# Performance work log

Measured on AMD Instinct MI355X. Metric: run time of the kernel, lower is better.

The kernel has to match this reference:

```python
import jax, jax.numpy as jnp
import numpy as np

DIM = 128

def setup_inputs() -> dict:
    key = jax.random.key(0)
    ks = jax.random.split(key, 4)
    N, C, L = 64, DIM, 4096
    scale = 1.0 / np.sqrt(DIM)
    return {
        "x": jax.random.normal(ks[0], (N, C, L), dtype=jnp.float32),
        "Wq": jax.random.normal(ks[1], (DIM, DIM), dtype=jnp.float32) * scale,
        "bq": jnp.zeros((DIM,), dtype=jnp.float32),
        "Wk": jax.random.normal(ks[2], (DIM, DIM), dtype=jnp.float32) * scale,
        "bk": jnp.zeros((DIM,), dtype=jnp.float32),
        "Wv": jax.random.normal(ks[3], (DIM, DIM), dtype=jnp.float32) * scale,
        "bv": jnp.zeros((DIM,), dtype=jnp.float32),
    }

def reference(x, Wq, bq, Wk, bk, Wv, bv):
    # x: [N, C, L] -> rearrange to [N, L, C]
    h = jnp.transpose(x, (0, 2, 1))                       # [N, L, C]
    q = jnp.einsum('nlc,cd->nld', h, Wq) + bq             # [N, L, D]
    k = jnp.einsum('nlc,cd->nld', h, Wk) + bk             # [N, L, D]
    v = jnp.einsum('nlc,cd->nld', h, Wv) + bv             # [N, L, D]
    # AFT-Simple: softmax over sequence axis of K, global weighted pool of V
    w = jax.nn.softmax(k, axis=1)                         # [N, L, D]
    pooled = jnp.sum(w * v, axis=1, keepdims=True)        # [N, 1, D]
    out = jax.nn.sigmoid(q) * pooled                      # [N, L, D]
    return jnp.transpose(out, (0, 2, 1))                  # [N, C, L]
```

## Files before the change

kernel.cpp:

```cpp
#include <hip/hip_runtime.h>
#include <hip/hip_bf16.h>

#define NB 64
#define CD 128
#define LL 4096
#define LCHUNK 64
#define NSUB 4
#define P1_NBLK 16
#define P3_NCHUNK 64

typedef __attribute__((ext_vector_type(8))) short short8;
typedef __attribute__((ext_vector_type(4))) float f32x4;

#define WT_OFF   0
#define WSM_OFF  131072
#define WSS_OFF  (WSM_OFF + NB*P1_NBLK*CD*4)
#define WSP_OFF  (WSS_OFF + NB*P1_NBLK*CD*4)
#define POOL_OFF (WSP_OFF + NB*P1_NBLK*CD*4)

__device__ __forceinline__ unsigned short f2bf(float f) {
    union { float f; unsigned u; } v; v.f = f;
    unsigned r = v.u + 0x7FFFu + ((v.u >> 16) & 1u);
    return (unsigned short)(r >> 16);
}

__global__ void prep_wt(const float* __restrict__ Wq, const float* __restrict__ Wk,
                        const float* __restrict__ Wv, unsigned short* __restrict__ wt) {
    int t = blockIdx.x >> 7;
    int d = blockIdx.x & 127;
    const float* W = (t == 0) ? Wq : (t == 1) ? Wk : Wv;
    int c = threadIdx.x;
    wt[((size_t)t*CD + d)*CD + c] = f2bf(W[c*CD + d]);
}

__global__ __launch_bounds__(256, 2)
void aft_pass1(const float* __restrict__ x, const unsigned short* __restrict__ wt,
               const float* __restrict__ bk, const float* __restrict__ bv,
               float* __restrict__ wsM, float* __restrict__ wsS, float* __restrict__ wsP) {
    __shared__ unsigned short lds_x[LCHUNK * 136];
    const int tid = threadIdx.x;
    const int n = blockIdx.x >> 4;
    const int blk = blockIdx.x & 15;
    const int w = tid >> 6, lane = tid & 63, r = lane & 15, g = lane >> 4;

    short8 a_k[2][4], a_v[2][4];
#pragma unroll
    for (int rt = 0; rt < 2; ++rt)
#pragma unroll
        for (int s = 0; s < 4; ++s) {
            int d = 32*w + 16*rt + r;
            a_k[rt][s] = *(const short8*)(wt + ((size_t)(1*CD + d))*CD + 32*s + 8*g);
            a_v[rt][s] = *(const short8*)(wt + ((size_t)(2*CD + d))*CD + 32*s + 8*g);
        }

    f32x4 bkv[2], bvv[2];
#pragma unroll
    for (int rt = 0; rt < 2; ++rt) {
        bkv[rt] = *(const f32x4*)(bk + 32*w + 16*rt + 4*g);
        bvv[rt] = *(const f32x4*)(bv + 32*w + 16*rt + 4*g);
    }

    float m_run[2][4], s_run[2][4], p_run[2][4];
#pragma unroll
    for (int rt = 0; rt < 2; ++rt)
#pragma unroll
        for (int v = 0; v < 4; ++v) { m_run[rt][v] = -1e30f; s_run[rt][v] = 0.f; p_run[rt][v] = 0.f; }

    for (int sub = 0; sub < NSUB; ++sub) {
        const int l0 = (blk*NSUB + sub) * LCHUNK;
        __syncthreads();
        {
            const int cc = tid >> 4, f = tid & 15;
#pragma unroll
            for (int it = 0; it < 8; ++it) {
                int c = cc + 16*it;
                f32x4 xv = *(const f32x4*)(x + ((size_t)n*CD + c)*LL + l0 + 4*f);
                int l = 4*f;
                lds_x[(l+0)*136 + c] = f2bf(xv[0]);
                lds_x[(l+1)*136 + c] = f2bf(xv[1]);
                lds_x[(l+2)*136 + c] = f2bf(xv[2]);
                lds_x[(l+3)*136 + c] = f2bf(xv[3]);
            }
        }
        __syncthreads();

        f32x4 acc_k[2][4], acc_v[2][4];
#pragma unroll
        for (int rt = 0; rt < 2; ++rt)
#pragma unroll
            for (int ct = 0; ct < 4; ++ct) {
                acc_k[rt][ct] = (f32x4){0.f,0.f,0.f,0.f};
                acc_v[rt][ct] = (f32x4){0.f,0.f,0.f,0.f};
            }

#pragma unroll
        for (int s = 0; s < 4; ++s) {
#pragma unroll
            for (int ct = 0; ct < 4; ++ct) {
                short8 b = *(const short8*)(lds_x + (ct*16 + r)*136 + 32*s + 8*g);
                acc_k[0][ct] = __builtin_amdgcn_mfma_f32_16x16x32_bf16(a_k[0][s], b, acc_k[0][ct], 0,0,0);
                acc_k[1][ct] = __builtin_amdgcn_mfma_f32_16x16x32_bf16(a_k[1][s], b, acc_k[1][ct], 0,0,0);
                acc_v[0][ct] = __builtin_amdgcn_mfma_f32_16x16x32_bf16(a_v[0][s], b, acc_v[0][ct], 0,0,0);
                acc_v[1][ct] = __builtin_amdgcn_mfma_f32_16x16x32_bf16(a_v[1][s], b, acc_v[1][ct], 0,0,0);
            }
        }

#pragma unroll
        for (int rt = 0; rt < 2; ++rt) {
#pragma unroll
            for (int v = 0; v < 4; ++v) {
                float k0 = acc_k[rt][0][v] + bkv[rt][v];
                float k1 = acc_k[rt][1][v] + bkv[rt][v];
                float k2 = acc_k[rt][2][v] + bkv[rt][v];
                float k3 = acc_k[rt][3][v] + bkv[rt][v];
                float v0 = acc_v[rt][0][v] + bvv[rt][v];
                float v1 = acc_v[rt][1][v] + bvv[rt][v];
                float v2 = acc_v[rt][2][v] + bvv[rt][v];
                float v3 = acc_v[rt][3][v] + bvv[rt][v];
                float m = fmaxf(fmaxf(k0,k1), fmaxf(k2,k3));
                m = fmaxf(m, __shfl_xor(m, 1, 64));
                m = fmaxf(m, __shfl_xor(m, 2, 64));
                m = fmaxf(m, __shfl_xor(m, 4, 64));
                m = fmaxf(m, __shfl_xor(m, 8, 64));
                float e0 = __expf(k0 - m), e1 = __expf(k1 - m);
                float e2 = __expf(k2 - m), e3 = __expf(k3 - m);
                float sl = (e0 + e1) + (e2 + e3);
                float pl = e0*v0 + e1*v1 + e2*v2 + e3*v3;
                sl += __shfl_xor(sl, 1, 64); pl += __shfl_xor(pl, 1, 64);
                sl += __shfl_xor(sl, 2, 64); pl += __shfl_xor(pl, 2, 64);
                sl += __shfl_xor(sl, 4, 64); pl += __shfl_xor(pl, 4, 64);
                sl += __shfl_xor(sl, 8, 64); pl += __shfl_xor(pl, 8, 64);
                float mo = m_run[rt][v];
                float mn = fmaxf(mo, m);
                float au = __expf(mo - mn);
                float bu = __expf(m - mn);
                s_run[rt][v] = s_run[rt][v]*au + sl*bu;
                p_run[rt][v] = p_run[rt][v]*au + pl*bu;
                m_run[rt][v] = mn;
            }
        }
    }

    if (r == 0) {
#pragma unroll
        for (int rt = 0; rt < 2; ++rt)
#pragma unroll
            for (int v = 0; v < 4; ++v) {
                int d = 32*w + 16*rt + 4*g + v;
                size_t idx = ((size_t)n*P1_NBLK + blk)*CD + d;
                wsM[idx] = m_run[rt][v];
                wsS[idx] = s_run[rt][v];
                wsP[idx] = p_run[rt][v];
            }
    }
}

__global__ void aft_pass2(const float* __restrict__ wsM, const float* __restrict__ wsS,
                          const float* __restrict__ wsP, float* __restrict__ pooled) {
    int n = blockIdx.x, d = threadIdx.x;
    float m = -1e30f, s = 0.f, p = 0.f;
    for (int b = 0; b < P1_NBLK; ++b) {
        size_t idx = ((size_t)n*P1_NBLK + b)*CD + d;
        float mb = wsM[idx], sb = wsS[idx], pb = wsP[idx];
        float mn = fmaxf(m, mb);
        float au = __expf(m - mn), bu = __expf(mb - mn);
        s = s*au + sb*bu;
        p = p*au + pb*bu;
        m = mn;
    }
    pooled[(size_t)n*CD + d] = p / s;
}

__global__ __launch_bounds__(256, 2)
void aft_pass3(const float* __restrict__ x, const unsigned short* __restrict__ wt,
               const float* __restrict__ bq, const float* __restrict__ pooled,
               float* __restrict__ out) {
    __shared__ unsigned short lds_x[LCHUNK * 136];
    __shared__ float lds_o[CD * 68];
    const int tid = threadIdx.x;
    const int n = blockIdx.x >> 6;
    const int ch = blockIdx.x & 63;
    const int l0 = ch * LCHUNK;
    const int w = tid >> 6, lane = tid & 63, r = lane & 15, g = lane >> 4;

    short8 a_q[2][4];
#pragma unroll
    for (int rt = 0; rt < 2; ++rt)
#pragma unroll
        for (int s = 0; s < 4; ++s) {
            int d = 32*w + 16*rt + r;
            a_q[rt][s] = *(const short8*)(wt + ((size_t)(0*CD + d))*CD + 32*s + 8*g);
        }

    {
        const int cc = tid >> 4, f = tid & 15;
#pragma unroll
        for (int it = 0; it < 8; ++it) {
            int c = cc + 16*it;
            f32x4 xv = *(const f32x4*)(x + ((size_t)n*CD + c)*LL + l0 + 4*f);
            int l = 4*f;
            lds_x[(l+0)*136 + c] = f2bf(xv[0]);
            lds_x[(l+1)*136 + c] = f2bf(xv[1]);
            lds_x[(l+2)*136 + c] = f2bf(xv[2]);
            lds_x[(l+3)*136 + c] = f2bf(xv[3]);
        }
    }
    __syncthreads();

    f32x4 acc[2][4];
#pragma unroll
    for (int rt = 0; rt < 2; ++rt)
#pragma unroll
        for (int ct = 0; ct < 4; ++ct) acc[rt][ct] = (f32x4){0.f,0.f,0.f,0.f};

#pragma unroll
    for (int s = 0; s < 4; ++s) {
#pragma unroll
        for (int ct = 0; ct < 4; ++ct) {
            short8 b = *(const short8*)(lds_x + (ct*16 + r)*136 + 32*s + 8*g);
            acc[0][ct] = __builtin_amdgcn_mfma_f32_16x16x32_bf16(a_q[0][s], b, acc[0][ct], 0,0,0);
            acc[1][ct] = __builtin_amdgcn_mfma_f32_16x16x32_bf16(a_q[1][s], b, acc[1][ct], 0,0,0);
        }
    }

    f32x4 bqv[2], plv[2];
#pragma unroll
    for (int rt = 0; rt < 2; ++rt) {
        bqv[rt] = *(const f32x4*)(bq + 32*w + 16*rt + 4*g);
        plv[rt] = *(const f32x4*)(pooled + (size_t)n*CD + 32*w + 16*rt + 4*g);
    }

#pragma unroll
    for (int rt = 0; rt < 2; ++rt)
#pragma unroll
        for (int ct = 0; ct < 4; ++ct)
#pragma unroll
            for (int v = 0; v < 4; ++v) {
                float q = acc[rt][ct][v] + bqv[rt][v];
                float o = plv[rt][v] / (1.f + __expf(-q));
                int d = 32*w + 16*rt + 4*g + v;
                lds_o[d*68 + ct*16 + r] = o;
            }
    __syncthreads();

    {
        const int f = tid & 15;
#pragma unroll
        for (int it = 0; it < 8; ++it) {
            int row = (tid >> 4) + 16*it;
            f32x4 val = *(const f32x4*)(lds_o + row*68 + 4*f);
            *(f32x4*)(out + ((size_t)n*CD + row)*LL + l0 + 4*f) = val;
        }
    }
}

extern "C" void kernel_launch(void* const* d_in, const int* in_sizes, int n_in,
                              void* d_out, int out_size, void* d_ws, size_t ws_size,
                              hipStream_t stream) {
    const float* x  = (const float*)d_in[0];
    const float* Wq = (const float*)d_in[1];
    const float* bq = (const float*)d_in[2];
    const float* Wk = (const float*)d_in[3];
    const float* bk = (const float*)d_in[4];
    const float* Wv = (const float*)d_in[5];
    const float* bv = (const float*)d_in[6];
    float* out = (float*)d_out;
    char* ws = (char*)d_ws;
    unsigned short* wt = (unsigned short*)(ws + WT_OFF);
    float* wsM = (float*)(ws + WSM_OFF);
    float* wsS = (float*)(ws + WSS_OFF);
    float* wsP = (float*)(ws + WSP_OFF);
    float* pooled = (float*)(ws + POOL_OFF);

    prep_wt<<<384, 128, 0, stream>>>(Wq, Wk, Wv, wt);
    aft_pass1<<<NB * P1_NBLK, 256, 0, stream>>>(x, wt, bk, bv, wsM, wsS, wsP);
    aft_pass2<<<NB, CD, 0, stream>>>(wsM, wsS, wsP, pooled);
    aft_pass3<<<NB * P3_NCHUNK, 256, 0, stream>>>(x, wt, bq, pooled, out);
}
```

Measured before the change: 106.2 us.

## Compute sigmoid(q) in pass1 as bf16 tile, make pass3 a scale-only stream

Pass1 now also computes the Q projection and stores sigmoid(q) as bf16 tiles in workspace, so pass3 no longer rereads x or runs a GEMM. Pass3 just multiplies each stored value by the pooled vector and writes fp32 output. The online softmax moves to exp2 with per-lane running state and a cross-lane merge only at the end, replacing the per-chunk shuffle reductions. The trade-off is an extra 64 MB bf16 write and read in place of the 128 MB fp32 reread of x, plus bf16 rounding of the sigmoid before the final multiply.

```diff
diff --git a/kernel.cpp b/kernel.cpp
--- a/kernel.cpp
+++ b/kernel.cpp
@@ -7,21 +7,28 @@
 #define LCHUNK 64
 #define NSUB 4
 #define P1_NBLK 16
-#define P3_NCHUNK 64
+#define NCHUNK 64
 
 typedef __attribute__((ext_vector_type(8))) short short8;
 typedef __attribute__((ext_vector_type(4))) float f32x4;
+
+#define LOG2E 1.4426950408889634f
 
 #define WT_OFF   0
 #define WSM_OFF  131072
 #define WSS_OFF  (WSM_OFF + NB*P1_NBLK*CD*4)
 #define WSP_OFF  (WSS_OFF + NB*P1_NBLK*CD*4)
 #define POOL_OFF (WSP_OFF + NB*P1_NBLK*CD*4)
+#define WSQ_OFF  (8u*1024u*1024u)
 
 __device__ __forceinline__ unsigned short f2bf(float f) {
     union { float f; unsigned u; } v; v.f = f;
     unsigned r = v.u + 0x7FFFu + ((v.u >> 16) & 1u);
     return (unsigned short)(r >> 16);
+}
+__device__ __forceinline__ float bf2f(unsigned short h) {
+    union { unsigned u; float f; } v; v.u = ((unsigned)h) << 16;
+    return v.f;
 }
 
 __global__ void prep_wt(const float* __restrict__ Wq, const float* __restrict__ Wk,
@@ -35,27 +42,32 @@
 
 __global__ __launch_bounds__(256, 2)
 void aft_pass1(const float* __restrict__ x, const unsigned short* __restrict__ wt,
-               const float* __restrict__ bk, const float* __restrict__ bv,
-               float* __restrict__ wsM, float* __restrict__ wsS, float* __restrict__ wsP) {
+               const float* __restrict__ bq, const float* __restrict__ bk,
+               const float* __restrict__ bv,
+               float* __restrict__ wsM, float* __restrict__ wsS, float* __restrict__ wsP,
+               unsigned short* __restrict__ wsq) {
     __shared__ unsigned short lds_x[LCHUNK * 136];
+    __shared__ unsigned short lds_q[CD * 68];
     const int tid = threadIdx.x;
     const int n = blockIdx.x >> 4;
     const int blk = blockIdx.x & 15;
     const int w = tid >> 6, lane = tid & 63, r = lane & 15, g = lane >> 4;
 
-    short8 a_k[2][4], a_v[2][4];
+    short8 a_q[2][4], a_k[2][4], a_v[2][4];
 #pragma unroll
     for (int rt = 0; rt < 2; ++rt)
 #pragma unroll
         for (int s = 0; s < 4; ++s) {
             int d = 32*w + 16*rt + r;
+            a_q[rt][s] = *(const short8*)(wt + ((size_t)(0*CD + d))*CD + 32*s + 8*g);
             a_k[rt][s] = *(const short8*)(wt + ((size_t)(1*CD + d))*CD + 32*s + 8*g);
             a_v[rt][s] = *(const short8*)(wt + ((size_t)(2*CD + d))*CD + 32*s + 8*g);
         }
 
-    f32x4 bkv[2], bvv[2];
+    f32x4 bqv[2], bkv[2], bvv[2];
 #pragma unroll
     for (int rt = 0; rt < 2; ++rt) {
+        bqv[rt] = *(const f32x4*)(bq + 32*w + 16*rt + 4*g);
         bkv[rt] = *(const f32x4*)(bk + 32*w + 16*rt + 4*g);
         bvv[rt] = *(const f32x4*)(bv + 32*w + 16*rt + 4*g);
     }
@@ -67,7 +79,8 @@
         for (int v = 0; v < 4; ++v) { m_run[rt][v] = -1e30f; s_run[rt][v] = 0.f; p_run[rt][v] = 0.f; }
 
     for (int sub = 0; sub < NSUB; ++sub) {
-        const int l0 = (blk*NSUB + sub) * LCHUNK;
+        const int ch = blk*NSUB + sub;
+        const int l0 = ch * LCHUNK;
         __syncthreads();
         {
             const int cc = tid >> 4, f = tid & 15;
@@ -84,62 +97,75 @@
         }
         __syncthreads();
 
-        f32x4 acc_k[2][4], acc_v[2][4];
-#pragma unroll
-        for (int rt = 0; rt < 2; ++rt)
-#pragma unroll
-            for (int ct = 0; ct < 4; ++ct) {
-                acc_k[rt][ct] = (f32x4){0.f,0.f,0.f,0.f};
-                acc_v[rt][ct] = (f32x4){0.f,0.f,0.f,0.f};
-            }
-
-#pragma unroll
-        for (int s = 0; s < 4; ++s) {
-#pragma unroll
-            for (int ct = 0; ct < 4; ++ct) {
+#pragma unroll
+        for (int ct = 0; ct < 4; ++ct) {
+            f32x4 aq[2], ak[2], av[2];
+#pragma unroll
+            for (int rt = 0; rt < 2; ++rt) {
+                aq[rt] = (f32x4){0.f,0.f,0.f,0.f};
+                ak[rt] = (f32x4){0.f,0.f,0.f,0.f};
+                av[rt] = (f32x4){0.f,0.f,0.f,0.f};
+            }
+#pragma unroll
+            for (int s = 0; s < 4; ++s) {
                 short8 b = *(const short8*)(lds_x + (ct*16 + r)*136 + 32*s + 8*g);
-                acc_k[0][ct] = __builtin_amdgcn_mfma_f32_16x16x32_bf16(a_k[0][s], b, acc_k[0][ct], 0,0,0);
-                acc_k[1][ct] = __builtin_amdgcn_mfma_f32_16x16x32_bf16(a_k[1][s], b, acc_k[1][ct], 0,0,0);
-                acc_v[0][ct] = __builtin_amdgcn_mfma_f32_16x16x32_bf16(a_v[0][s], b, acc_v[0][ct], 0,0,0);
-                acc_v[1][ct] = __builtin_amdgcn_mfma_f32_16x16x32_bf16(a_v[1][s], b, acc_v[1][ct], 0,0,0);
-            }
-        }
-
-#pragma unroll
-        for (int rt = 0; rt < 2; ++rt) {
-#pragma unroll
-            for (int v = 0; v < 4; ++v) {
-                float k0 = acc_k[rt][0][v] + bkv[rt][v];
-                float k1 = acc_k[rt][1][v] + bkv[rt][v];
-                float k2 = acc_k[rt][2][v] + bkv[rt][v];
-                float k3 = acc_k[rt][3][v] + bkv[rt][v];
-                float v0 = acc_v[rt][0][v] + bvv[rt][v];
-                float v1 = acc_v[rt][1][v] + bvv[rt][v];
-                float v2 = acc_v[rt][2][v] + bvv[rt][v];
-                float v3 = acc_v[rt][3][v] + bvv[rt][v];
-                float m = fmaxf(fmaxf(k0,k1), fmaxf(k2,k3));
-                m = fmaxf(m, __shfl_xor(m, 1, 64));
-                m = fmaxf(m, __shfl_xor(m, 2, 64));
-                m = fmaxf(m, __shfl_xor(m, 4, 64));
-                m = fmaxf(m, __shfl_xor(m, 8, 64));
-                float e0 = __expf(k0 - m), e1 = __expf(k1 - m);
-                float e2 = __expf(k2 - m), e3 = __expf(k3 - m);
-                float sl = (e0 + e1) + (e2 + e3);
-                float pl = e0*v0 + e1*v1 + e2*v2 + e3*v3;
-                sl += __shfl_xor(sl, 1, 64); pl += __shfl_xor(pl, 1, 64);
-                sl += __shfl_xor(sl, 2, 64); pl += __shfl_xor(pl, 2, 64);
-                sl += __shfl_xor(sl, 4, 64); pl += __shfl_xor(pl, 4, 64);
-                sl += __shfl_xor(sl, 8, 64); pl += __shfl_xor(pl, 8, 64);
-                float mo = m_run[rt][v];
-                float mn = fmaxf(mo, m);
-                float au = __expf(mo - mn);
-                float bu = __expf(m - mn);
-                s_run[rt][v] = s_run[rt][v]*au + sl*bu;
-                p_run[rt][v] = p_run[rt][v]*au + pl*bu;
-                m_run[rt][v] = mn;
-            }
-        }
-    }
+                aq[0] = __builtin_amdgcn_mfma_f32_16x16x32_bf16(a_q[0][s], b, aq[0], 0,0,0);
+                aq[1] = __builtin_amdgcn_mfma_f32_16x16x32_bf16(a_q[1][s], b, aq[1], 0,0,0);
+                ak[0] = __builtin_amdgcn_mfma_f32_16x16x32_bf16(a_k[0][s], b, ak[0], 0,0,0);
+                ak[1] = __builtin_amdgcn_mfma_f32_16x16x32_bf16(a_k[1][s], b, ak[1], 0,0,0);
+                av[0] = __builtin_amdgcn_mfma_f32_16x16x32_bf16(a_v[0][s], b, av[0], 0,0,0);
+                av[1] = __builtin_amdgcn_mfma_f32_16x16x32_bf16(a_v[1][s], b, av[1], 0,0,0);
+            }
+#pragma unroll
+            for (int rt = 0; rt < 2; ++rt)
+#pragma unroll
+                for (int v = 0; v < 4; ++v) {
+                    float k2 = (ak[rt][v] + bkv[rt][v]) * LOG2E;
+                    float vv = av[rt][v] + bvv[rt][v];
+                    float mo = m_run[rt][v];
+                    float mn = fmaxf(mo, k2);
+                    float sc = __builtin_amdgcn_exp2f(mo - mn);
+                    float e  = __builtin_amdgcn_exp2f(k2 - mn);
+                    s_run[rt][v] = s_run[rt][v]*sc + e;
+                    p_run[rt][v] = p_run[rt][v]*sc + e*vv;
+                    m_run[rt][v] = mn;
+                    float q2 = (aq[rt][v] + bqv[rt][v]) * LOG2E;
+                    float sg = __builtin_amdgcn_rcpf(1.f + __builtin_amdgcn_exp2f(-q2));
+                    lds_q[(32*w + 16*rt + 4*g + v)*68 + ct*16 + r] = f2bf(sg);
+                }
+        }
+        __syncthreads();
+        {
+            unsigned short* tile = wsq + ((size_t)(n*NCHUNK + ch)) * (CD*LCHUNK);
+            const int col = tid & 7;
+#pragma unroll
+            for (int it = 0; it < 4; ++it) {
+                int row = (tid >> 3) + 32*it;
+                short8 val = *(const short8*)(lds_q + row*68 + 8*col);
+                *(short8*)(tile + row*LCHUNK + 8*col) = val;
+            }
+        }
+    }
+
+#pragma unroll
+    for (int rt = 0; rt < 2; ++rt)
+#pragma unroll
+        for (int v = 0; v < 4; ++v) {
+            float m = m_run[rt][v], s = s_run[rt][v], p = p_run[rt][v];
+#pragma unroll
+            for (int mask = 1; mask <= 8; mask <<= 1) {
+                float om = __shfl_xor(m, mask, 64);
+                float os = __shfl_xor(s, mask, 64);
+                float op = __shfl_xor(p, mask, 64);
+                float mn = fmaxf(m, om);
+                float sc1 = __builtin_amdgcn_exp2f(m - mn);
+                float sc2 = __builtin_amdgcn_exp2f(om - mn);
+                s = s*sc1 + os*sc2;
+                p = p*sc1 + op*sc2;
+                m = mn;
+            }
+            m_run[rt][v] = m; s_run[rt][v] = s; p_run[rt][v] = p;
+        }
 
     if (r == 0) {
 #pragma unroll
@@ -163,7 +189,8 @@
         size_t idx = ((size_t)n*P1_NBLK + b)*CD + d;
         float mb = wsM[idx], sb = wsS[idx], pb = wsP[idx];
         float mn = fmaxf(m, mb);
-        float au = __expf(m - mn), bu = __expf(mb - mn);
+        float au = __builtin_amdgcn_exp2f(m - mn);
+        float bu = __builtin_amdgcn_exp2f(mb - mn);
         s = s*au + sb*bu;
         p = p*au + pb*bu;
         m = mn;
@@ -171,86 +198,31 @@
     pooled[(size_t)n*CD + d] = p / s;
 }
 
-__global__ __launch_bounds__(256, 2)
-void aft_pass3(const float* __restrict__ x, const unsigned short* __restrict__ wt,
-               const float* __restrict__ bq, const float* __restrict__ pooled,
+__global__ __launch_bounds__(256)
+void aft_pass3(const unsigned short* __restrict__ wsq, const float* __restrict__ pooled,
                float* __restrict__ out) {
-    __shared__ unsigned short lds_x[LCHUNK * 136];
-    __shared__ float lds_o[CD * 68];
-    const int tid = threadIdx.x;
+    __shared__ float lpool[CD];
     const int n = blockIdx.x >> 6;
     const int ch = blockIdx.x & 63;
+    if (threadIdx.x < CD) lpool[threadIdx.x] = pooled[(size_t)n*CD + threadIdx.x];
+    __syncthreads();
+    const unsigned short* tile = wsq + ((size_t)(n*NCHUNK + ch)) * (CD*LCHUNK);
     const int l0 = ch * LCHUNK;
-    const int w = tid >> 6, lane = tid & 63, r = lane & 15, g = lane >> 4;
-
-    short8 a_q[2][4];
-#pragma unroll
-    for (int rt = 0; rt < 2; ++rt)
-#pragma unroll
-        for (int s = 0; s < 4; ++s) {
-            int d = 32*w + 16*rt + r;
-            a_q[rt][s] = *(const short8*)(wt + ((size_t)(0*CD + d))*CD + 32*s + 8*g);
-        }
-
-    {
-        const int cc = tid >> 4, f = tid & 15;
-#pragma unroll
-        for (int it = 0; it < 8; ++it) {
-            int c = cc + 16*it;
-            f32x4 xv = *(const f32x4*)(x + ((size_t)n*CD + c)*LL + l0 + 4*f);
-            int l = 4*f;
-            lds_x[(l+0)*136 + c] = f2bf(xv[0]);
-            lds_x[(l+1)*136 + c] = f2bf(xv[1]);
-            lds_x[(l+2)*136 + c] = f2bf(xv[2]);
-            lds_x[(l+3)*136 + c] = f2bf(xv[3]);
-        }
-    }
-    __syncthreads();
-
-    f32x4 acc[2][4];
-#pragma unroll
-    for (int rt = 0; rt < 2; ++rt)
-#pragma unroll
-        for (int ct = 0; ct < 4; ++ct) acc[rt][ct] = (f32x4){0.f,0.f,0.f,0.f};
-
-#pragma unroll
-    for (int s = 0; s < 4; ++s) {
-#pragma unroll
-        for (int ct = 0; ct < 4; ++ct) {
-            short8 b = *(const short8*)(lds_x + (ct*16 + r)*136 + 32*s + 8*g);
-            acc[0][ct] = __builtin_amdgcn_mfma_f32_16x16x32_bf16(a_q[0][s], b, acc[0][ct], 0,0,0);
-            acc[1][ct] = __builtin_amdgcn_mfma_f32_16x16x32_bf16(a_q[1][s], b, acc[1][ct], 0,0,0);
-        }
-    }
-
-    f32x4 bqv[2], plv[2];
-#pragma unroll
-    for (int rt = 0; rt < 2; ++rt) {
-        bqv[rt] = *(const f32x4*)(bq + 32*w + 16*rt + 4*g);
-        plv[rt] = *(const f32x4*)(pooled + (size_t)n*CD + 32*w + 16*rt + 4*g);
-    }
-
-#pragma unroll
-    for (int rt = 0; rt < 2; ++rt)
-#pragma unroll
-        for (int ct = 0; ct < 4; ++ct)
-#pragma unroll
-            for (int v = 0; v < 4; ++v) {
-                float q = acc[rt][ct][v] + bqv[rt][v];
-                float o = plv[rt][v] / (1.f + __expf(-q));
-                int d = 32*w + 16*rt + 4*g + v;
-                lds_o[d*68 + ct*16 + r] = o;
-            }
-    __syncthreads();
-
-    {
-        const int f = tid & 15;
-#pragma unroll
-        for (int it = 0; it < 8; ++it) {
-            int row = (tid >> 4) + 16*it;
-            f32x4 val = *(const f32x4*)(lds_o + row*68 + 4*f);
-            *(f32x4*)(out + ((size_t)n*CD + row)*LL + l0 + 4*f) = val;
-        }
+#pragma unroll
+    for (int it = 0; it < 4; ++it) {
+        int gi = threadIdx.x + 256*it;
+        int row = gi >> 3, col = gi & 7;
+        short8 v = *(const short8*)(tile + row*LCHUNK + 8*col);
+        float pl = lpool[row];
+        f32x4 o0, o1;
+#pragma unroll
+        for (int j = 0; j < 4; ++j) {
+            o0[j] = bf2f((unsigned short)v[j]) * pl;
+            o1[j] = bf2f((unsigned short)v[4+j]) * pl;
+        }
+        float* dst = out + ((size_t)n*CD + row)*LL + l0 + 8*col;
+        *(f32x4*)dst = o0;
+        *(f32x4*)(dst + 4) = o1;
     }
 }
 
@@ -271,9 +243,10 @@
     float* wsS = (float*)(ws + WSS_OFF);
     float* wsP = (float*)(ws + WSP_OFF);
     float* pooled = (float*)(ws + POOL_OFF);
+    unsigned short* wsq = (unsigned short*)(ws + WSQ_OFF);
 
     prep_wt<<<384, 128, 0, stream>>>(Wq, Wk, Wv, wt);
-    aft_pass1<<<NB * P1_NBLK, 256, 0, stream>>>(x, wt, bk, bv, wsM, wsS, wsP);
+    aft_pass1<<<NB * P1_NBLK, 256, 0, stream>>>(x, wt, bq, bk, bv, wsM, wsS, wsP, wsq);
     aft_pass2<<<NB, CD, 0, stream>>>(wsM, wsS, wsP, pooled);
-    aft_pass3<<<NB * P3_NCHUNK, 256, 0, stream>>>(x, wt, bq, pooled, out);
-}
+    aft_pass3<<<NB * NCHUNK, 256, 0, stream>>>(wsq, pooled, out);
+}
```

After: 131.9 us. 24.2% more time.
